# Performance work log

Measured on AMD Instinct MI355X. Metric: run time of the kernel, lower is better.

The kernel has to match this reference:

```python
import jax, jax.numpy as jnp
import numpy as np

D_MODEL = 1024
NUM_HEADS = 16
HEAD_WIDTH = 64
SEQ_LEN = 2048
BATCH = 2
NEG_INF = -1e9


def alibi_slopes(num_heads):
    # 2**(-i * 8/num_heads) for i = 1..num_heads, shape [H, 1, 1]
    step = 8.0 / num_heads
    i = jnp.arange(1, num_heads + 1, dtype=jnp.float32)
    return (2.0 ** (-i * step))[:, None, None]


def relative_positions(t_q, t_v):
    # matrix[i, j] = j - i, shape [t_q, t_v]
    return (jnp.arange(t_v)[None, :] - jnp.arange(t_q)[:, None]).astype(jnp.float32)


def setup_inputs() -> dict:
    key = jax.random.key(0)
    ks = jax.random.split(key, 6)
    queries = jax.random.normal(ks[0], (BATCH, SEQ_LEN, D_MODEL), dtype=jnp.float32)
    keys = jax.random.normal(ks[1], (BATCH, SEQ_LEN, D_MODEL), dtype=jnp.float32)
    values = jax.random.normal(ks[2], (BATCH, SEQ_LEN, D_MODEL), dtype=jnp.float32)
    # causal additive mask, broadcastable [1, 1, S, S]
    causal = jnp.where(
        jnp.arange(SEQ_LEN)[None, :] > jnp.arange(SEQ_LEN)[:, None], NEG_INF, 0.0
    ).astype(jnp.float32)[None, None]
    scale = 1.0 / np.sqrt(D_MODEL)
    Wq = jax.random.normal(ks[3], (D_MODEL, D_MODEL), dtype=jnp.float32) * scale
    Wk = jax.random.normal(ks[4], (D_MODEL, D_MODEL), dtype=jnp.float32) * scale
    Wv = jax.random.normal(ks[5], (D_MODEL, D_MODEL), dtype=jnp.float32) * scale
    return {"queries": queries, "keys": keys, "values": values, "mask": causal,
            "Wq": Wq, "Wk": Wk, "Wv": Wv}


def reference(queries, keys, values, mask, Wq, Wk, Wv):
    N, t_q, d = queries.shape
    _, t_v, _ = keys.shape
    H, hw = NUM_HEADS, HEAD_WIDTH

    def split_heads(x, t):
        # [N, t, d] -> [N, H, t, hw]  (nn.Linear: x @ W.T)
        return x.reshape(N, t, H, hw).transpose(0, 2, 1, 3)

    q = split_heads(queries @ Wq.T, t_q)
    k = split_heads(keys @ Wk.T, t_v)
    v = split_heads(values @ Wv.T, t_v)

    att = jnp.einsum("bhqd,bhkd->bhqk", q, k) / np.sqrt(hw)
    # ALiBi bias: slope_h * (j - i), broadcast over batch
    att = att + (alibi_slopes(H) * relative_positions(t_q, t_v))[None]
    att = att + mask[:, :, :t_q, :t_v]
    att = jax.nn.softmax(att, axis=-1)
    res = jnp.einsum("bhqk,bhkd->bhqd", att, v)  # [N, H, t_q, hw]
    return res.transpose(0, 2, 1, 3).reshape(N, t_v, d)
```

## Files before the change

kernel.cpp:

```cpp
#include <hip/hip_runtime.h>
#include <hip/hip_bf16.h>

#define BATCH 2
#define HEADS 16
#define SEQ 2048
#define HW 64
#define DMODEL 1024

typedef unsigned short u16;
typedef __attribute__((ext_vector_type(8))) short short8;
typedef __attribute__((ext_vector_type(4))) float floatx4;

__device__ __forceinline__ u16 f2bf(float f) {
    union { float f; unsigned int u; } v; v.f = f;
    unsigned int r = v.u + 0x7fffu + ((v.u >> 16) & 1u);
    return (u16)(r >> 16);
}

__device__ __forceinline__ unsigned int pk2bf(float a, float b) {
    union { __hip_bfloat162 h; unsigned int u; } c;
    c.h = __float22bfloat162_rn(make_float2(a, b));
    return c.u;
}

__global__ __launch_bounds__(256) void proj_kernel(
    const float* __restrict__ Xk, const float* __restrict__ Xv,
    const float* __restrict__ Wk, const float* __restrict__ Wv,
    u16* __restrict__ Ok, u16* __restrict__ Ov)
{
    const float* X; const float* W;
    if (blockIdx.z == 0) { X = Xk; W = Wk; }
    else                 { X = Xv; W = Wv; }

    __shared__ u16 As[128][72];
    __shared__ u16 Bs[128][72];

    const int tid = threadIdx.x;
    const int lane = tid & 63, wave = tid >> 6;
    const int quad = lane >> 4, l15 = lane & 15;
    const int wm = (wave >> 1) << 6, wn = (wave & 1) << 6;
    const int tm = blockIdx.y, tn = blockIdx.x;

    const int sr = tid >> 4;
    const int sc = (tid & 15) << 2;
    const float* Xp = X + (size_t)(tm * 128 + sr) * DMODEL + sc;
    const float* Wp = W + (size_t)(tn * 128 + sr) * DMODEL + sc;

    float4 ra[8], rb[8];
#define PLOAD(K0) \
    for (int i = 0; i < 8; i++) { \
        ra[i] = *reinterpret_cast<const float4*>(Xp + (size_t)16 * i * DMODEL + (K0)); \
        rb[i] = *reinterpret_cast<const float4*>(Wp + (size_t)16 * i * DMODEL + (K0)); \
    }

    floatx4 acc[4][4];
    for (int i = 0; i < 4; i++) for (int j = 0; j < 4; j++) acc[i][j] = (floatx4)0.0f;

    PLOAD(0);
    for (int k0 = 0; k0 < DMODEL; k0 += 64) {
        for (int i = 0; i < 8; i++) {
            uint2 pa; pa.x = pk2bf(ra[i].x, ra[i].y); pa.y = pk2bf(ra[i].z, ra[i].w);
            *reinterpret_cast<uint2*>(&As[sr + 16 * i][sc]) = pa;
            uint2 pb; pb.x = pk2bf(rb[i].x, rb[i].y); pb.y = pk2bf(rb[i].z, rb[i].w);
            *reinterpret_cast<uint2*>(&Bs[sr + 16 * i][sc]) = pb;
        }
        __syncthreads();
        if (k0 + 64 < DMODEL) { PLOAD(k0 + 64); }
        for (int kc = 0; kc < 2; kc++) {
            short8 af[4], bf[4];
            for (int i = 0; i < 4; i++)
                af[i] = *reinterpret_cast<const short8*>(&As[wm + i * 16 + l15][kc * 32 + quad * 8]);
            for (int j = 0; j < 4; j++)
                bf[j] = *reinterpret_cast<const short8*>(&Bs[wn + j * 16 + l15][kc * 32 + quad * 8]);
            for (int i = 0; i < 4; i++)
                for (int j = 0; j < 4; j++)
                    acc[i][j] = __builtin_amdgcn_mfma_f32_16x16x32_bf16(af[i], bf[j], acc[i][j], 0, 0, 0);
        }
        __syncthreads();
    }
#undef PLOAD

    if (blockIdx.z == 0) {
        for (int i = 0; i < 4; i++) for (int j = 0; j < 4; j++) {
            int n = (tn << 7) + wn + (j << 4) + l15;
            int h = n >> 6, d = n & 63;
            for (int r = 0; r < 4; r++) {
                int m = (tm << 7) + wm + (i << 4) + (quad << 2) + r;
                int b = m >> 11, s = m & 2047;
                Ok[(size_t)((((b << 4) + h) << 11) + s) * 64 + d] = f2bf(acc[i][j][r]);
            }
        }
    } else {
        for (int i = 0; i < 4; i++) for (int j = 0; j < 4; j++) {
            int n = (tn << 7) + wn + (j << 4) + l15;
            int h = n >> 6, d = n & 63;
            int m = (tm << 7) + wm + (i << 4) + (quad << 2);
            int b = m >> 11, s0 = m & 2047;
            uint2 pk;
            pk.x = pk2bf(acc[i][j][0], acc[i][j][1]);
            pk.y = pk2bf(acc[i][j][2], acc[i][j][3]);
            *reinterpret_cast<uint2*>(Ov + ((size_t)(((b << 4) + h) << 6) + d) * SEQ + s0) = pk;
        }
    }
}

__global__ __launch_bounds__(256) void attn_kernel(
    const float* __restrict__ Xq, const float* __restrict__ Wq,
    const u16* __restrict__ K, const u16* __restrict__ VtG,
    float* __restrict__ out)
{
    __shared__ u16 smem[3][64][72];

    const int tid = threadIdx.x;
    const int lane = tid & 63, wave = tid >> 6;
    const int quad = lane >> 4, l15 = lane & 15;

    const int bid = blockIdx.x;
    const int qt = 31 - (bid >> 5);
    const int bh = bid & 31;
    const int b = bh >> 4, h = bh & 15;
    const float slope = exp2f(-0.5f * (float)(h + 1));
    const int q0 = qt << 6;

    const u16* Kh  = K   + (size_t)bh * SEQ * HW;
    const u16* Vth = VtG + (size_t)bh * HW * SEQ;

    const int sr8 = tid >> 3, sc8 = (tid & 7) << 3;
    short8 pk0, pk1, pv0, pv1;
#define KVLOAD(KV) \
    pk0 = *reinterpret_cast<const short8*>(Kh + (size_t)((KV) + sr8) * 64 + sc8); \
    pk1 = *reinterpret_cast<const short8*>(Kh + (size_t)((KV) + sr8 + 32) * 64 + sc8); \
    pv0 = *reinterpret_cast<const short8*>(Vth + (size_t)sr8 * SEQ + (KV) + sc8); \
    pv1 = *reinterpret_cast<const short8*>(Vth + (size_t)(sr8 + 32) * SEQ + (KV) + sc8);

    KVLOAD(0);

    {
        const float* Xb = Xq + (size_t)b * SEQ * DMODEL;
        const float* Wh = Wq + (size_t)h * 64 * DMODEL;
        const int qsr = tid >> 4, qsc = (tid & 15) << 2;
        const float* Xp = Xb + (size_t)(q0 + qsr) * DMODEL + qsc;
        const float* Wp = Wh + (size_t)qsr * DMODEL + qsc;
        float4 qa[4], qw[4];
#define QLOAD(K0) \
        for (int i = 0; i < 4; i++) { \
            qa[i] = *reinterpret_cast<const float4*>(Xp + (size_t)16 * i * DMODEL + (K0)); \
            qw[i] = *reinterpret_cast<const float4*>(Wp + (size_t)16 * i * DMODEL + (K0)); \
        }
        floatx4 accq[4];
        for (int t = 0; t < 4; t++) accq[t] = (floatx4)0.0f;

        QLOAD(0);
        for (int k0 = 0; k0 < DMODEL; k0 += 64) {
            for (int i = 0; i < 4; i++) {
                uint2 pa; pa.x = pk2bf(qa[i].x, qa[i].y); pa.y = pk2bf(qa[i].z, qa[i].w);
                *reinterpret_cast<uint2*>(&smem[0][qsr + 16 * i][qsc]) = pa;
                uint2 pw; pw.x = pk2bf(qw[i].x, qw[i].y); pw.y = pk2bf(qw[i].z, qw[i].w);
                *reinterpret_cast<uint2*>(&smem[1][qsr + 16 * i][qsc]) = pw;
            }
            __syncthreads();
            if (k0 + 64 < DMODEL) { QLOAD(k0 + 64); }
            for (int kc = 0; kc < 2; kc++) {
                short8 xa = *reinterpret_cast<const short8*>(&smem[0][wave * 16 + l15][kc * 32 + quad * 8]);
                for (int tn = 0; tn < 4; tn++) {
                    short8 wb = *reinterpret_cast<const short8*>(&smem[1][tn * 16 + l15][kc * 32 + quad * 8]);
                    accq[tn] = __builtin_amdgcn_mfma_f32_16x16x32_bf16(xa, wb, accq[tn], 0, 0, 0);
                }
            }
            __syncthreads();
        }
#undef QLOAD
        for (int tn = 0; tn < 4; tn++)
            for (int r = 0; r < 4; r++)
                smem[2][wave * 16 + (quad << 2) + r][tn * 16 + l15] = f2bf(accq[tn][r] * 0.125f);
    }
    short8 qf[2];
    qf[0] = *reinterpret_cast<const short8*>(&smem[2][wave * 16 + l15][quad * 8]);
    qf[1] = *reinterpret_cast<const short8*>(&smem[2][wave * 16 + l15][32 + quad * 8]);
    __syncthreads();

    u16 (*Ks)[72] = smem[0];
    u16 (*Vt)[72] = smem[1];
    u16 (*Pt)[72] = &smem[2][wave * 16];

    const float L2E = 1.44269504088896340736f;
    const float MB  = 12.0f * L2E;
    const int qg = q0 + (wave << 4) + l15;
    const float SL = slope * L2E;

    float lpart = 0.0f;
    floatx4 acc_o[4];
    for (int t = 0; t < 4; t++) acc_o[t] = (floatx4)0.0f;

    for (int kt = 0; kt <= qt; kt++) {
        const int kv0 = kt << 6;
        *reinterpret_cast<short8*>(&Ks[sr8][sc8])      = pk0;
        *reinterpret_cast<short8*>(&Ks[sr8 + 32][sc8]) = pk1;
        *reinterpret_cast<short8*>(&Vt[sr8][sc8])      = pv0;
        *reinterpret_cast<short8*>(&Vt[sr8 + 32][sc8]) = pv1;
        __syncthreads();
        if (kt < qt) { KVLOAD(kv0 + 64); }

        floatx4 sv[4];
        for (int t = 0; t < 4; t++) {
            short8 kf0 = *reinterpret_cast<const short8*>(&Ks[t * 16 + l15][quad * 8]);
            short8 kf1 = *reinterpret_cast<const short8*>(&Ks[t * 16 + l15][32 + quad * 8]);
            floatx4 s = (floatx4)0.0f;
            s = __builtin_amdgcn_mfma_f32_16x16x32_bf16(kf0, qf[0], s, 0, 0, 0);
            s = __builtin_amdgcn_mfma_f32_16x16x32_bf16(kf1, qf[1], s, 0, 0, 0);
            sv[t] = s;
        }

        const float b0 = fmaf(SL, (float)(kv0 + (quad << 2) - qg), -MB);
        if (kt < qt) {
            for (int t = 0; t < 4; t++) {
                float p0 = __builtin_amdgcn_exp2f(fmaf(sv[t][0], L2E, fmaf(SL, (float)(t * 16 + 0), b0)));
                float p1 = __builtin_amdgcn_exp2f(fmaf(sv[t][1], L2E, fmaf(SL, (float)(t * 16 + 1), b0)));
                float p2 = __builtin_amdgcn_exp2f(fmaf(sv[t][2], L2E, fmaf(SL, (float)(t * 16 + 2), b0)));
                float p3 = __builtin_amdgcn_exp2f(fmaf(sv[t][3], L2E, fmaf(SL, (float)(t * 16 + 3), b0)));
                lpart += (p0 + p1) + (p2 + p3);
                uint2 pk; pk.x = pk2bf(p0, p1); pk.y = pk2bf(p2, p3);
                *reinterpret_cast<uint2*>(&Pt[l15][t * 16 + (quad << 2)]) = pk;
            }
        } else {
            const float fbase = (float)(kv0 + (quad << 2) - qg);
            for (int t = 0; t < 4; t++) {
                float p[4];
                for (int r = 0; r < 4; r++) {
                    float rel = fbase + (float)(t * 16 + r);
                    float bd = fmaf(fminf(slope * rel, -1e9f * rel), L2E, -MB);
                    p[r] = __builtin_amdgcn_exp2f(fmaf(sv[t][r], L2E, bd));
                }
                lpart += (p[0] + p[1]) + (p[2] + p[3]);
                uint2 pk; pk.x = pk2bf(p[0], p[1]); pk.y = pk2bf(p[2], p[3]);
                *reinterpret_cast<uint2*>(&Pt[l15][t * 16 + (quad << 2)]) = pk;
            }
        }

        for (int c = 0; c < 2; c++) {
            short8 pf = *reinterpret_cast<const short8*>(&Pt[l15][c * 32 + quad * 8]);
            for (int t2 = 0; t2 < 4; t2++) {
                short8 vf = *reinterpret_cast<const short8*>(&Vt[t2 * 16 + l15][c * 32 + quad * 8]);
                acc_o[t2] = __builtin_amdgcn_mfma_f32_16x16x32_bf16(vf, pf, acc_o[t2], 0, 0, 0);
            }
        }
        __syncthreads();
    }
#undef KVLOAD

    float l_run = lpart;
    l_run += __shfl_xor(l_run, 16);
    l_run += __shfl_xor(l_run, 32);
    const float inv = 1.0f / l_run;

    float* op = out + (size_t)(b * SEQ + qg) * DMODEL + h * 64;
    for (int t2 = 0; t2 < 4; t2++) {
        float4 o;
        o.x = acc_o[t2][0] * inv; o.y = acc_o[t2][1] * inv;
        o.z = acc_o[t2][2] * inv; o.w = acc_o[t2][3] * inv;
        *reinterpret_cast<float4*>(op + t2 * 16 + (quad << 2)) = o;
    }
}

extern "C" void kernel_launch(void* const* d_in, const int* in_sizes, int n_in,
                              void* d_out, int out_size, void* d_ws, size_t ws_size,
                              hipStream_t stream) {
    const float* q  = (const float*)d_in[0];
    const float* k  = (const float*)d_in[1];
    const float* v  = (const float*)d_in[2];
    const float* wq = (const float*)d_in[4];
    const float* wk = (const float*)d_in[5];
    const float* wv = (const float*)d_in[6];
    float* out = (float*)d_out;

    const size_t headElems = (size_t)BATCH * HEADS * SEQ * HW;
    u16* Kb  = (u16*)d_ws;
    u16* VtB = Kb + headElems;

    dim3 pgrid(DMODEL / 128, (BATCH * SEQ) / 128, 2);
    proj_kernel<<<pgrid, 256, 0, stream>>>(k, v, wk, wv, Kb, VtB);
    attn_kernel<<<BATCH * HEADS * (SEQ / 64), 256, 0, stream>>>(q, wq, Kb, VtB, out);
}
```

Baseline: 212.9 us.

## Double attention query tile to 128 rows per block, each wave owning 32 rows

Each attention block now handles 128 query rows instead of 64, with every wave computing two 16-row groups. K/V tiles loaded into shared memory are reused across twice as many queries, and the fused Q projection reuses each Wq tile across 128 rows. Waves whose rows lie entirely before a KV tile skip that tile's work. The cost is fewer blocks (512 vs 1024), more registers per thread, and more causal imbalance between waves inside a block.

```diff
diff --git a/kernel.cpp b/kernel.cpp
--- a/kernel.cpp
+++ b/kernel.cpp
@@ -109,18 +109,18 @@
     const u16* __restrict__ K, const u16* __restrict__ VtG,
     float* __restrict__ out)
 {
-    __shared__ u16 smem[3][64][72];
+    __shared__ u16 smem[256][72];
 
     const int tid = threadIdx.x;
     const int lane = tid & 63, wave = tid >> 6;
     const int quad = lane >> 4, l15 = lane & 15;
 
     const int bid = blockIdx.x;
-    const int qt = 31 - (bid >> 5);
+    const int qt = 15 - (bid >> 5);
     const int bh = bid & 31;
     const int b = bh >> 4, h = bh & 15;
     const float slope = exp2f(-0.5f * (float)(h + 1));
-    const int q0 = qt << 6;
+    const int q0 = qt << 7;
 
     const u16* Kh  = K   + (size_t)bh * SEQ * HW;
     const u16* Vth = VtG + (size_t)bh * HW * SEQ;
@@ -141,124 +141,148 @@
         const int qsr = tid >> 4, qsc = (tid & 15) << 2;
         const float* Xp = Xb + (size_t)(q0 + qsr) * DMODEL + qsc;
         const float* Wp = Wh + (size_t)qsr * DMODEL + qsc;
-        float4 qa[4], qw[4];
+        float4 qa[8], qw[4];
 #define QLOAD(K0) \
-        for (int i = 0; i < 4; i++) { \
+        for (int i = 0; i < 8; i++) \
             qa[i] = *reinterpret_cast<const float4*>(Xp + (size_t)16 * i * DMODEL + (K0)); \
-            qw[i] = *reinterpret_cast<const float4*>(Wp + (size_t)16 * i * DMODEL + (K0)); \
-        }
-        floatx4 accq[4];
-        for (int t = 0; t < 4; t++) accq[t] = (floatx4)0.0f;
+        for (int i = 0; i < 4; i++) \
+            qw[i] = *reinterpret_cast<const float4*>(Wp + (size_t)16 * i * DMODEL + (K0));
+        floatx4 accq[2][4];
+        for (int mg = 0; mg < 2; mg++) for (int t = 0; t < 4; t++) accq[mg][t] = (floatx4)0.0f;
 
         QLOAD(0);
         for (int k0 = 0; k0 < DMODEL; k0 += 64) {
+            for (int i = 0; i < 8; i++) {
+                uint2 pa; pa.x = pk2bf(qa[i].x, qa[i].y); pa.y = pk2bf(qa[i].z, qa[i].w);
+                *reinterpret_cast<uint2*>(&smem[qsr + 16 * i][qsc]) = pa;
+            }
             for (int i = 0; i < 4; i++) {
-                uint2 pa; pa.x = pk2bf(qa[i].x, qa[i].y); pa.y = pk2bf(qa[i].z, qa[i].w);
-                *reinterpret_cast<uint2*>(&smem[0][qsr + 16 * i][qsc]) = pa;
                 uint2 pw; pw.x = pk2bf(qw[i].x, qw[i].y); pw.y = pk2bf(qw[i].z, qw[i].w);
-                *reinterpret_cast<uint2*>(&smem[1][qsr + 16 * i][qsc]) = pw;
+                *reinterpret_cast<uint2*>(&smem[128 + qsr + 16 * i][qsc]) = pw;
             }
             __syncthreads();
             if (k0 + 64 < DMODEL) { QLOAD(k0 + 64); }
             for (int kc = 0; kc < 2; kc++) {
-                short8 xa = *reinterpret_cast<const short8*>(&smem[0][wave * 16 + l15][kc * 32 + quad * 8]);
-                for (int tn = 0; tn < 4; tn++) {
-                    short8 wb = *reinterpret_cast<const short8*>(&smem[1][tn * 16 + l15][kc * 32 + quad * 8]);
-                    accq[tn] = __builtin_amdgcn_mfma_f32_16x16x32_bf16(xa, wb, accq[tn], 0, 0, 0);
-                }
+                short8 af[2], bf[4];
+                for (int mg = 0; mg < 2; mg++)
+                    af[mg] = *reinterpret_cast<const short8*>(&smem[wave * 32 + mg * 16 + l15][kc * 32 + quad * 8]);
+                for (int t = 0; t < 4; t++)
+                    bf[t] = *reinterpret_cast<const short8*>(&smem[128 + t * 16 + l15][kc * 32 + quad * 8]);
+                for (int mg = 0; mg < 2; mg++)
+                    for (int t = 0; t < 4; t++)
+                        accq[mg][t] = __builtin_amdgcn_mfma_f32_16x16x32_bf16(af[mg], bf[t], accq[mg][t], 0, 0, 0);
             }
             __syncthreads();
         }
 #undef QLOAD
-        for (int tn = 0; tn < 4; tn++)
-            for (int r = 0; r < 4; r++)
-                smem[2][wave * 16 + (quad << 2) + r][tn * 16 + l15] = f2bf(accq[tn][r] * 0.125f);
-    }
-    short8 qf[2];
-    qf[0] = *reinterpret_cast<const short8*>(&smem[2][wave * 16 + l15][quad * 8]);
-    qf[1] = *reinterpret_cast<const short8*>(&smem[2][wave * 16 + l15][32 + quad * 8]);
-    __syncthreads();
-
-    u16 (*Ks)[72] = smem[0];
-    u16 (*Vt)[72] = smem[1];
-    u16 (*Pt)[72] = &smem[2][wave * 16];
+        const int sb = 128 + wave * 32;
+        for (int mg = 0; mg < 2; mg++)
+            for (int t = 0; t < 4; t++)
+                for (int r = 0; r < 4; r++)
+                    smem[sb + mg * 16 + (quad << 2) + r][t * 16 + l15] = f2bf(accq[mg][t][r] * 0.125f);
+    }
+    short8 qf[2][2];
+    for (int g = 0; g < 2; g++)
+        for (int c = 0; c < 2; c++)
+            qf[g][c] = *reinterpret_cast<const short8*>(&smem[128 + wave * 32 + g * 16 + l15][c * 32 + quad * 8]);
+
+    u16 (*Pt)[72] = &smem[128 + wave * 32];
 
     const float L2E = 1.44269504088896340736f;
     const float MB  = 12.0f * L2E;
-    const int qg = q0 + (wave << 4) + l15;
-    const float SL = slope * L2E;
-
-    float lpart = 0.0f;
-    floatx4 acc_o[4];
-    for (int t = 0; t < 4; t++) acc_o[t] = (floatx4)0.0f;
-
-    for (int kt = 0; kt <= qt; kt++) {
+    const float SL  = slope * L2E;
+    const int wqmin = q0 + wave * 32;
+    const int ktmax_w = (wqmin + 31) >> 6;
+    const int ktend   = (q0 + 127) >> 6;
+
+    float lpart[2] = {0.0f, 0.0f};
+    floatx4 acc_o[2][4];
+    for (int g = 0; g < 2; g++) for (int t = 0; t < 4; t++) acc_o[g][t] = (floatx4)0.0f;
+
+    for (int kt = 0; kt <= ktend; kt++) {
         const int kv0 = kt << 6;
-        *reinterpret_cast<short8*>(&Ks[sr8][sc8])      = pk0;
-        *reinterpret_cast<short8*>(&Ks[sr8 + 32][sc8]) = pk1;
-        *reinterpret_cast<short8*>(&Vt[sr8][sc8])      = pv0;
-        *reinterpret_cast<short8*>(&Vt[sr8 + 32][sc8]) = pv1;
+        *reinterpret_cast<short8*>(&smem[sr8][sc8])       = pk0;
+        *reinterpret_cast<short8*>(&smem[sr8 + 32][sc8])  = pk1;
+        *reinterpret_cast<short8*>(&smem[64 + sr8][sc8])  = pv0;
+        *reinterpret_cast<short8*>(&smem[96 + sr8][sc8])  = pv1;
         __syncthreads();
-        if (kt < qt) { KVLOAD(kv0 + 64); }
-
-        floatx4 sv[4];
-        for (int t = 0; t < 4; t++) {
-            short8 kf0 = *reinterpret_cast<const short8*>(&Ks[t * 16 + l15][quad * 8]);
-            short8 kf1 = *reinterpret_cast<const short8*>(&Ks[t * 16 + l15][32 + quad * 8]);
-            floatx4 s = (floatx4)0.0f;
-            s = __builtin_amdgcn_mfma_f32_16x16x32_bf16(kf0, qf[0], s, 0, 0, 0);
-            s = __builtin_amdgcn_mfma_f32_16x16x32_bf16(kf1, qf[1], s, 0, 0, 0);
-            sv[t] = s;
-        }
-
-        const float b0 = fmaf(SL, (float)(kv0 + (quad << 2) - qg), -MB);
-        if (kt < qt) {
+        if (kt < ktend) { KVLOAD(kv0 + 64); }
+
+        if (kt <= ktmax_w) {
+            short8 kf[4][2];
             for (int t = 0; t < 4; t++) {
-                float p0 = __builtin_amdgcn_exp2f(fmaf(sv[t][0], L2E, fmaf(SL, (float)(t * 16 + 0), b0)));
-                float p1 = __builtin_amdgcn_exp2f(fmaf(sv[t][1], L2E, fmaf(SL, (float)(t * 16 + 1), b0)));
-                float p2 = __builtin_amdgcn_exp2f(fmaf(sv[t][2], L2E, fmaf(SL, (float)(t * 16 + 2), b0)));
-                float p3 = __builtin_amdgcn_exp2f(fmaf(sv[t][3], L2E, fmaf(SL, (float)(t * 16 + 3), b0)));
-                lpart += (p0 + p1) + (p2 + p3);
-                uint2 pk; pk.x = pk2bf(p0, p1); pk.y = pk2bf(p2, p3);
-                *reinterpret_cast<uint2*>(&Pt[l15][t * 16 + (quad << 2)]) = pk;
-            }
-        } else {
-            const float fbase = (float)(kv0 + (quad << 2) - qg);
-            for (int t = 0; t < 4; t++) {
-                float p[4];
-                for (int r = 0; r < 4; r++) {
-                    float rel = fbase + (float)(t * 16 + r);
-                    float bd = fmaf(fminf(slope * rel, -1e9f * rel), L2E, -MB);
-                    p[r] = __builtin_amdgcn_exp2f(fmaf(sv[t][r], L2E, bd));
+                kf[t][0] = *reinterpret_cast<const short8*>(&smem[t * 16 + l15][quad * 8]);
+                kf[t][1] = *reinterpret_cast<const short8*>(&smem[t * 16 + l15][32 + quad * 8]);
+            }
+            const bool masked = (kv0 + 63) > wqmin;
+
+            for (int g = 0; g < 2; g++) {
+                floatx4 sv[4];
+                for (int t = 0; t < 4; t++) {
+                    floatx4 s = (floatx4)0.0f;
+                    s = __builtin_amdgcn_mfma_f32_16x16x32_bf16(kf[t][0], qf[g][0], s, 0, 0, 0);
+                    s = __builtin_amdgcn_mfma_f32_16x16x32_bf16(kf[t][1], qf[g][1], s, 0, 0, 0);
+                    sv[t] = s;
                 }
-                lpart += (p[0] + p[1]) + (p[2] + p[3]);
-                uint2 pk; pk.x = pk2bf(p[0], p[1]); pk.y = pk2bf(p[2], p[3]);
-                *reinterpret_cast<uint2*>(&Pt[l15][t * 16 + (quad << 2)]) = pk;
-            }
-        }
-
-        for (int c = 0; c < 2; c++) {
-            short8 pf = *reinterpret_cast<const short8*>(&Pt[l15][c * 32 + quad * 8]);
+                const int qg_ = wqmin + g * 16 + l15;
+                if (!masked) {
+                    const float b0 = fmaf(SL, (float)(kv0 + (quad << 2) - qg_), -MB);
+                    for (int t = 0; t < 4; t++) {
+                        float p0 = __builtin_amdgcn_exp2f(fmaf(sv[t][0], L2E, fmaf(SL, (float)(t * 16 + 0), b0)));
+                        float p1 = __builtin_amdgcn_exp2f(fmaf(sv[t][1], L2E, fmaf(SL, (float)(t * 16 + 1), b0)));
+                        float p2 = __builtin_amdgcn_exp2f(fmaf(sv[t][2], L2E, fmaf(SL, (float)(t * 16 + 2), b0)));
+                        float p3 = __builtin_amdgcn_exp2f(fmaf(sv[t][3], L2E, fmaf(SL, (float)(t * 16 + 3), b0)));
+                        lpart[g] += (p0 + p1) + (p2 + p3);
+                        uint2 pk; pk.x = pk2bf(p0, p1); pk.y = pk2bf(p2, p3);
+                        *reinterpret_cast<uint2*>(&Pt[g * 16 + l15][t * 16 + (quad << 2)]) = pk;
+                    }
+                } else {
+                    const float fb = (float)(kv0 + (quad << 2) - qg_);
+                    for (int t = 0; t < 4; t++) {
+                        float p[4];
+                        for (int r = 0; r < 4; r++) {
+                            float rel = fb + (float)(t * 16 + r);
+                            float bd = fmaf(fminf(slope * rel, -1e9f * rel), L2E, -MB);
+                            p[r] = __builtin_amdgcn_exp2f(fmaf(sv[t][r], L2E, bd));
+                        }
+                        lpart[g] += (p[0] + p[1]) + (p[2] + p[3]);
+                        uint2 pk; pk.x = pk2bf(p[0], p[1]); pk.y = pk2bf(p[2], p[3]);
+                        *reinterpret_cast<uint2*>(&Pt[g * 16 + l15][t * 16 + (quad << 2)]) = pk;
+                    }
+                }
+            }
+
+            short8 vf[4][2];
             for (int t2 = 0; t2 < 4; t2++) {
-                short8 vf = *reinterpret_cast<const short8*>(&Vt[t2 * 16 + l15][c * 32 + quad * 8]);
-                acc_o[t2] = __builtin_amdgcn_mfma_f32_16x16x32_bf16(vf, pf, acc_o[t2], 0, 0, 0);
+                vf[t2][0] = *reinterpret_cast<const short8*>(&smem[64 + t2 * 16 + l15][quad * 8]);
+                vf[t2][1] = *reinterpret_cast<const short8*>(&smem[64 + t2 * 16 + l15][32 + quad * 8]);
+            }
+            for (int g = 0; g < 2; g++) {
+                short8 pf0 = *reinterpret_cast<const short8*>(&Pt[g * 16 + l15][quad * 8]);
+                short8 pf1 = *reinterpret_cast<const short8*>(&Pt[g * 16 + l15][32 + quad * 8]);
+                for (int t2 = 0; t2 < 4; t2++) {
+                    acc_o[g][t2] = __builtin_amdgcn_mfma_f32_16x16x32_bf16(vf[t2][0], pf0, acc_o[g][t2], 0, 0, 0);
+                    acc_o[g][t2] = __builtin_amdgcn_mfma_f32_16x16x32_bf16(vf[t2][1], pf1, acc_o[g][t2], 0, 0, 0);
+                }
             }
         }
         __syncthreads();
     }
 #undef KVLOAD
 
-    float l_run = lpart;
-    l_run += __shfl_xor(l_run, 16);
-    l_run += __shfl_xor(l_run, 32);
-    const float inv = 1.0f / l_run;
-
-    float* op = out + (size_t)(b * SEQ + qg) * DMODEL + h * 64;
-    for (int t2 = 0; t2 < 4; t2++) {
-        float4 o;
-        o.x = acc_o[t2][0] * inv; o.y = acc_o[t2][1] * inv;
-        o.z = acc_o[t2][2] * inv; o.w = acc_o[t2][3] * inv;
-        *reinterpret_cast<float4*>(op + t2 * 16 + (quad << 2)) = o;
+    for (int g = 0; g < 2; g++) {
+        float l = lpart[g];
+        l += __shfl_xor(l, 16);
+        l += __shfl_xor(l, 32);
+        const float inv = 1.0f / l;
+        const int qg_ = wqmin + g * 16 + l15;
+        float* op = out + (size_t)(b * SEQ + qg_) * DMODEL + h * 64;
+        for (int t2 = 0; t2 < 4; t2++) {
+            float4 o;
+            o.x = acc_o[g][t2][0] * inv; o.y = acc_o[g][t2][1] * inv;
+            o.z = acc_o[g][t2][2] * inv; o.w = acc_o[g][t2][3] * inv;
+            *reinterpret_cast<float4*>(op + t2 * 16 + (quad << 2)) = o;
+        }
     }
 }
 
@@ -279,5 +303,5 @@
 
     dim3 pgrid(DMODEL / 128, (BATCH * SEQ) / 128, 2);
     proj_kernel<<<pgrid, 256, 0, stream>>>(k, v, wk, wv, Kb, VtB);
-    attn_kernel<<<BATCH * HEADS * (SEQ / 64), 256, 0, stream>>>(q, wq, Kb, VtB, out);
-}
+    attn_kernel<<<BATCH * HEADS * (SEQ / 128), 256, 0, stream>>>(q, wq, Kb, VtB, out);
+}
```

New measurement: 217.3 us. 2.0% more time.

## Load K/V tiles directly into LDS with swizzled layout and double-buffered K

Applied to the files above, without the earlier changes.

The projection kernel now writes K and V^T in an XOR-swizzled column order, so the attention kernel can stream them into LDS with global_load_lds instead of staging through registers. K is double-buffered across iterations. V is loaded within the same iteration, overlapping with the QK^T and softmax work, and a second vmcnt wait plus barrier precedes the PV MFMAs. The aim is lower register pressure and fewer VGPR-to-LDS store instructions while keeping LDS reads conflict-free via the swizzle. The trade-off is an extra barrier per tile and V latency that is only partly hidden.

```diff
diff --git a/kernel.cpp b/kernel.cpp
--- a/kernel.cpp
+++ b/kernel.cpp
@@ -10,6 +10,9 @@
 typedef unsigned short u16;
 typedef __attribute__((ext_vector_type(8))) short short8;
 typedef __attribute__((ext_vector_type(4))) float floatx4;
+
+typedef __attribute__((address_space(3))) void* lds_t;
+typedef const __attribute__((address_space(1))) void* gbl_t;
 
 __device__ __forceinline__ u16 f2bf(float f) {
     union { float f; unsigned int u; } v; v.f = f;
@@ -87,7 +90,8 @@
             for (int r = 0; r < 4; r++) {
                 int m = (tm << 7) + wm + (i << 4) + (quad << 2) + r;
                 int b = m >> 11, s = m & 2047;
-                Ok[(size_t)((((b << 4) + h) << 11) + s) * 64 + d] = f2bf(acc[i][j][r]);
+                int pc = (((d >> 3) ^ (s & 7)) << 3) | (d & 7);
+                Ok[(size_t)((((b << 4) + h) << 11) + s) * 64 + pc] = f2bf(acc[i][j][r]);
             }
         }
     } else {
@@ -96,10 +100,11 @@
             int h = n >> 6, d = n & 63;
             int m = (tm << 7) + wm + (i << 4) + (quad << 2);
             int b = m >> 11, s0 = m & 2047;
+            int ps = (s0 & ~63) | (((((s0 >> 3) & 7) ^ (d & 7)) << 3)) | (s0 & 7);
             uint2 pk;
             pk.x = pk2bf(acc[i][j][0], acc[i][j][1]);
             pk.y = pk2bf(acc[i][j][2], acc[i][j][3]);
-            *reinterpret_cast<uint2*>(Ov + ((size_t)(((b << 4) + h) << 6) + d) * SEQ + s0) = pk;
+            *reinterpret_cast<uint2*>(Ov + ((size_t)(((b << 4) + h) << 6) + d) * SEQ + ps) = pk;
         }
     }
 }
@@ -109,7 +114,8 @@
     const u16* __restrict__ K, const u16* __restrict__ VtG,
     float* __restrict__ out)
 {
-    __shared__ u16 smem[3][64][72];
+    __shared__ u16 smem[16896];
+    u16* Pst = smem + 12288;
 
     const int tid = threadIdx.x;
     const int lane = tid & 63, wave = tid >> 6;
@@ -125,17 +131,20 @@
     const u16* Kh  = K   + (size_t)bh * SEQ * HW;
     const u16* Vth = VtG + (size_t)bh * HW * SEQ;
 
-    const int sr8 = tid >> 3, sc8 = (tid & 7) << 3;
-    short8 pk0, pk1, pv0, pv1;
-#define KVLOAD(KV) \
-    pk0 = *reinterpret_cast<const short8*>(Kh + (size_t)((KV) + sr8) * 64 + sc8); \
-    pk1 = *reinterpret_cast<const short8*>(Kh + (size_t)((KV) + sr8 + 32) * 64 + sc8); \
-    pv0 = *reinterpret_cast<const short8*>(Vth + (size_t)sr8 * SEQ + (KV) + sc8); \
-    pv1 = *reinterpret_cast<const short8*>(Vth + (size_t)(sr8 + 32) * SEQ + (KV) + sc8);
-
-    KVLOAD(0);
+#define ISSUE_K(KV, BUF) do { \
+    const u16* gk_ = Kh + (size_t)((KV) + wave * 16) * 64 + lane * 8; \
+    __builtin_amdgcn_global_load_lds((gbl_t)gk_, (lds_t)(smem + (BUF) * 4096 + wave * 1024), 16, 0, 0); \
+    __builtin_amdgcn_global_load_lds((gbl_t)(gk_ + 512), (lds_t)(smem + (BUF) * 4096 + wave * 1024 + 512), 16, 0, 0); \
+} while (0)
+#define ISSUE_V(KV) do { \
+    const u16* gv_ = Vth + (size_t)(wave * 16 + (lane >> 3)) * SEQ + (KV) + (lane & 7) * 8; \
+    __builtin_amdgcn_global_load_lds((gbl_t)gv_, (lds_t)(smem + 8192 + wave * 1024), 16, 0, 0); \
+    __builtin_amdgcn_global_load_lds((gbl_t)(gv_ + 8 * SEQ), (lds_t)(smem + 8192 + wave * 1024 + 512), 16, 0, 0); \
+} while (0)
 
     {
+        u16 (*As)[72] = reinterpret_cast<u16(*)[72]>(smem);
+        u16 (*Bs)[72] = reinterpret_cast<u16(*)[72]>(smem + 4608);
         const float* Xb = Xq + (size_t)b * SEQ * DMODEL;
         const float* Wh = Wq + (size_t)h * 64 * DMODEL;
         const int qsr = tid >> 4, qsc = (tid & 15) << 2;
@@ -154,16 +163,16 @@
         for (int k0 = 0; k0 < DMODEL; k0 += 64) {
             for (int i = 0; i < 4; i++) {
                 uint2 pa; pa.x = pk2bf(qa[i].x, qa[i].y); pa.y = pk2bf(qa[i].z, qa[i].w);
-                *reinterpret_cast<uint2*>(&smem[0][qsr + 16 * i][qsc]) = pa;
+                *reinterpret_cast<uint2*>(&As[qsr + 16 * i][qsc]) = pa;
                 uint2 pw; pw.x = pk2bf(qw[i].x, qw[i].y); pw.y = pk2bf(qw[i].z, qw[i].w);
-                *reinterpret_cast<uint2*>(&smem[1][qsr + 16 * i][qsc]) = pw;
+                *reinterpret_cast<uint2*>(&Bs[qsr + 16 * i][qsc]) = pw;
             }
             __syncthreads();
             if (k0 + 64 < DMODEL) { QLOAD(k0 + 64); }
             for (int kc = 0; kc < 2; kc++) {
-                short8 xa = *reinterpret_cast<const short8*>(&smem[0][wave * 16 + l15][kc * 32 + quad * 8]);
+                short8 xa = *reinterpret_cast<const short8*>(&As[wave * 16 + l15][kc * 32 + quad * 8]);
                 for (int tn = 0; tn < 4; tn++) {
-                    short8 wb = *reinterpret_cast<const short8*>(&smem[1][tn * 16 + l15][kc * 32 + quad * 8]);
+                    short8 wb = *reinterpret_cast<const short8*>(&Bs[tn * 16 + l15][kc * 32 + quad * 8]);
                     accq[tn] = __builtin_amdgcn_mfma_f32_16x16x32_bf16(xa, wb, accq[tn], 0, 0, 0);
                 }
             }
@@ -172,21 +181,19 @@
 #undef QLOAD
         for (int tn = 0; tn < 4; tn++)
             for (int r = 0; r < 4; r++)
-                smem[2][wave * 16 + (quad << 2) + r][tn * 16 + l15] = f2bf(accq[tn][r] * 0.125f);
+                Pst[wave * 1152 + ((quad << 2) + r) * 72 + tn * 16 + l15] = f2bf(accq[tn][r] * 0.125f);
     }
     short8 qf[2];
-    qf[0] = *reinterpret_cast<const short8*>(&smem[2][wave * 16 + l15][quad * 8]);
-    qf[1] = *reinterpret_cast<const short8*>(&smem[2][wave * 16 + l15][32 + quad * 8]);
-    __syncthreads();
-
-    u16 (*Ks)[72] = smem[0];
-    u16 (*Vt)[72] = smem[1];
-    u16 (*Pt)[72] = &smem[2][wave * 16];
+    qf[0] = *reinterpret_cast<const short8*>(Pst + wave * 1152 + l15 * 72 + quad * 8);
+    qf[1] = *reinterpret_cast<const short8*>(Pst + wave * 1152 + l15 * 72 + 32 + quad * 8);
+
+    ISSUE_K(0, 0);
 
     const float L2E = 1.44269504088896340736f;
     const float MB  = 12.0f * L2E;
     const int qg = q0 + (wave << 4) + l15;
     const float SL = slope * L2E;
+    const int swz = l15 & 7;
 
     float lpart = 0.0f;
     floatx4 acc_o[4];
@@ -194,25 +201,25 @@
 
     for (int kt = 0; kt <= qt; kt++) {
         const int kv0 = kt << 6;
-        *reinterpret_cast<short8*>(&Ks[sr8][sc8])      = pk0;
-        *reinterpret_cast<short8*>(&Ks[sr8 + 32][sc8]) = pk1;
-        *reinterpret_cast<short8*>(&Vt[sr8][sc8])      = pv0;
-        *reinterpret_cast<short8*>(&Vt[sr8 + 32][sc8]) = pv1;
-        __syncthreads();
-        if (kt < qt) { KVLOAD(kv0 + 64); }
-
+        asm volatile("s_waitcnt vmcnt(0)" ::: "memory");
+        __syncthreads();
+        if (kt < qt) { ISSUE_K(kv0 + 64, (kt + 1) & 1); }
+        ISSUE_V(kv0);
+
+        const u16* Kbase = smem + (kt & 1) * 4096;
         floatx4 sv[4];
         for (int t = 0; t < 4; t++) {
-            short8 kf0 = *reinterpret_cast<const short8*>(&Ks[t * 16 + l15][quad * 8]);
-            short8 kf1 = *reinterpret_cast<const short8*>(&Ks[t * 16 + l15][32 + quad * 8]);
+            short8 kf0 = *reinterpret_cast<const short8*>(Kbase + (t * 16 + l15) * 64 + ((quad ^ swz) << 3));
+            short8 kf1 = *reinterpret_cast<const short8*>(Kbase + (t * 16 + l15) * 64 + (((quad + 4) ^ swz) << 3));
             floatx4 s = (floatx4)0.0f;
             s = __builtin_amdgcn_mfma_f32_16x16x32_bf16(kf0, qf[0], s, 0, 0, 0);
             s = __builtin_amdgcn_mfma_f32_16x16x32_bf16(kf1, qf[1], s, 0, 0, 0);
             sv[t] = s;
         }
 
-        const float b0 = fmaf(SL, (float)(kv0 + (quad << 2) - qg), -MB);
+        u16* Pt = Pst + wave * 1152;
         if (kt < qt) {
+            const float b0 = fmaf(SL, (float)(kv0 + (quad << 2) - qg), -MB);
             for (int t = 0; t < 4; t++) {
                 float p0 = __builtin_amdgcn_exp2f(fmaf(sv[t][0], L2E, fmaf(SL, (float)(t * 16 + 0), b0)));
                 float p1 = __builtin_amdgcn_exp2f(fmaf(sv[t][1], L2E, fmaf(SL, (float)(t * 16 + 1), b0)));
@@ -220,33 +227,37 @@
                 float p3 = __builtin_amdgcn_exp2f(fmaf(sv[t][3], L2E, fmaf(SL, (float)(t * 16 + 3), b0)));
                 lpart += (p0 + p1) + (p2 + p3);
                 uint2 pk; pk.x = pk2bf(p0, p1); pk.y = pk2bf(p2, p3);
-                *reinterpret_cast<uint2*>(&Pt[l15][t * 16 + (quad << 2)]) = pk;
+                *reinterpret_cast<uint2*>(Pt + l15 * 72 + t * 16 + (quad << 2)) = pk;
             }
         } else {
-            const float fbase = (float)(kv0 + (quad << 2) - qg);
+            const float fb = (float)(kv0 + (quad << 2) - qg);
             for (int t = 0; t < 4; t++) {
                 float p[4];
                 for (int r = 0; r < 4; r++) {
-                    float rel = fbase + (float)(t * 16 + r);
+                    float rel = fb + (float)(t * 16 + r);
                     float bd = fmaf(fminf(slope * rel, -1e9f * rel), L2E, -MB);
                     p[r] = __builtin_amdgcn_exp2f(fmaf(sv[t][r], L2E, bd));
                 }
                 lpart += (p[0] + p[1]) + (p[2] + p[3]);
                 uint2 pk; pk.x = pk2bf(p[0], p[1]); pk.y = pk2bf(p[2], p[3]);
-                *reinterpret_cast<uint2*>(&Pt[l15][t * 16 + (quad << 2)]) = pk;
-            }
-        }
-
-        for (int c = 0; c < 2; c++) {
-            short8 pf = *reinterpret_cast<const short8*>(&Pt[l15][c * 32 + quad * 8]);
-            for (int t2 = 0; t2 < 4; t2++) {
-                short8 vf = *reinterpret_cast<const short8*>(&Vt[t2 * 16 + l15][c * 32 + quad * 8]);
-                acc_o[t2] = __builtin_amdgcn_mfma_f32_16x16x32_bf16(vf, pf, acc_o[t2], 0, 0, 0);
-            }
-        }
-        __syncthreads();
-    }
-#undef KVLOAD
+                *reinterpret_cast<uint2*>(Pt + l15 * 72 + t * 16 + (quad << 2)) = pk;
+            }
+        }
+
+        asm volatile("s_waitcnt vmcnt(0)" ::: "memory");
+        __syncthreads();
+
+        short8 pf0 = *reinterpret_cast<const short8*>(Pt + l15 * 72 + quad * 8);
+        short8 pf1 = *reinterpret_cast<const short8*>(Pt + l15 * 72 + 32 + quad * 8);
+        for (int t2 = 0; t2 < 4; t2++) {
+            short8 vf0 = *reinterpret_cast<const short8*>(smem + 8192 + (t2 * 16 + l15) * 64 + ((quad ^ swz) << 3));
+            short8 vf1 = *reinterpret_cast<const short8*>(smem + 8192 + (t2 * 16 + l15) * 64 + (((quad + 4) ^ swz) << 3));
+            acc_o[t2] = __builtin_amdgcn_mfma_f32_16x16x32_bf16(vf0, pf0, acc_o[t2], 0, 0, 0);
+            acc_o[t2] = __builtin_amdgcn_mfma_f32_16x16x32_bf16(vf1, pf1, acc_o[t2], 0, 0, 0);
+        }
+    }
+#undef ISSUE_K
+#undef ISSUE_V
 
     float l_run = lpart;
     l_run += __shfl_xor(l_run, 16);
```

New measurement: 208.6 us. 2.0% less time.
